# Kernel tuning notes

Hardware: AMD Instinct MI355X
Metric: run time of the kernel (lower is better)

The kernel has to match this reference:

```python
import jax, jax.numpy as jnp
import numpy as np

N, PAIR, M, D, O, R = 4096, 2, 64, 128, 128, 2
MAX_DEG = 32


def setup_inputs() -> dict:
    key = jax.random.key(0)
    k1, k2, k3, k4, k5, k6 = jax.random.split(key, 6)
    node_features = jax.random.normal(k1, (N, PAIR, M, D), dtype=jnp.float32)
    deg = jax.random.randint(k2, (N,), 0, MAX_DEG, dtype=jnp.int32)
    # per-relation Linear params (stored as [in, out]) and self-loop Linear
    W_r = jax.random.normal(k3, (R, D, O), dtype=jnp.float32) / np.sqrt(D)
    b_r = jax.random.normal(k4, (R, O), dtype=jnp.float32) * 0.01
    W0 = jax.random.normal(k5, (D, O), dtype=jnp.float32) / np.sqrt(D)
    b0 = jax.random.normal(k6, (O,), dtype=jnp.float32) * 0.01
    return {"node_features": node_features, "deg": deg, "W_r": W_r,
            "b_r": b_r, "W0": W0, "b0": b0}


def reference(node_features, deg, W_r, b_r, W0, b0):
    # Original: for each relation r, for each neighbor, adds W_r(x_i);
    # i.e. sum_r deg_i * (x_i @ W_r + b_r) = deg_i * (x_i @ sum_r W_r + sum_r b_r)
    Wsum = W_r.sum(axis=0)          # [D, O]
    bsum = b_r.sum(axis=0)          # [O]
    rel = jnp.einsum('npmd,do->npmo', node_features, Wsum) + bsum
    self_term = jnp.einsum('npmd,do->npmo', node_features, W0) + b0
    d = deg.astype(node_features.dtype)[:, None, None, None]
    h = jax.nn.relu(d * rel + self_term)  # [N, 2, M, O]
    # edge representation: mm(h_i, h_j.T) per entity -> [N, M, M]
    out = jnp.einsum('nmo,nko->nmk', h[:, 0], h[:, 1])
    return out
```

## Files before the change

kernel.cpp:

```cpp
#include <hip/hip_runtime.h>
#include <hip/hip_bf16.h>


typedef __attribute__((ext_vector_type(8))) short bf16x8;
typedef __attribute__((ext_vector_type(4))) float f32x4;

__device__ __forceinline__ unsigned int pkbf(float a, float b) {
    union { __hip_bfloat162 h; unsigned int u; } v;
    v.h = __float22bfloat162_rn(float2{a, b});
    return v.u;
}

__global__ __launch_bounds__(256) void build_weights(
    const float* __restrict__ W_r,
    const float* __restrict__ b_r,
    const float* __restrict__ W0,
    const float* __restrict__ b0,
    unsigned short* __restrict__ wfrag,
    float* __restrict__ call)
{
    int t = blockIdx.x * blockDim.x + threadIdx.x;
    int lane = t & 63;
    int ks = (t >> 6) & 3;
    int ct = (t >> 8) & 7;
    int d  = (t >> 11) & 31;
    int o = ct * 16 + (lane & 15);
    int kbase = ks * 32 + (lane >> 4) * 8;
    unsigned int* dst = (unsigned int*)(wfrag + (size_t)t * 8);
#pragma unroll
    for (int j = 0; j < 4; ++j) {
        int k0 = kbase + 2 * j;
        float wA = (float)d * (W_r[k0 * 128 + o] + W_r[128 * 128 + k0 * 128 + o]) + W0[k0 * 128 + o];
        float wB = (float)d * (W_r[(k0 + 1) * 128 + o] + W_r[128 * 128 + (k0 + 1) * 128 + o]) + W0[(k0 + 1) * 128 + o];
        dst[j] = pkbf(wA, wB);
    }
    if (t < 32 * 128) {
        int dd = t >> 7, oo = t & 127;
        call[t] = (float)dd * (b_r[oo] + b_r[128 + oo]) + b0[oo];
    }
}

__global__ __launch_bounds__(256) void edge_kernel(
    const float* __restrict__ x,
    const int* __restrict__ deg,
    const unsigned short* __restrict__ wfrag,
    const float* __restrict__ call,
    float* __restrict__ out)
{
    __shared__ unsigned short hlds[16384];
    char* const ldsb = (char*)hlds;

    const int n = blockIdx.x;
    const int tid = threadIdx.x;
    const int wave = tid >> 6;
    const int lane = tid & 63;
    const int l15 = lane & 15;
    const int lhi = lane >> 4;
    const int d = deg[n];

    const float* xn = x + (size_t)n * (2 * 64 * 128);
    const char* wsrc = (const char*)(wfrag + (size_t)d * (8 * 4 * 64 * 8));
    const float* cd = call + d * 128;

    f32x4 wst[8];
#pragma unroll
    for (int i = 0; i < 8; ++i)
        wst[i] = *(const f32x4*)(wsrc + i * 4096 + tid * 16);

    const int rbase = wave * 32;
    bf16x8 afrag[2][4];
    f32x4 xraw[2][4][2];
#pragma unroll
    for (int rt = 0; rt < 2; ++rt) {
        const float* rowp = xn + (size_t)(rbase + rt * 16 + l15) * 128;
#pragma unroll
        for (int ks = 0; ks < 4; ++ks) {
            const f32x4* p = (const f32x4*)(rowp + ks * 32 + lhi * 8);
            xraw[rt][ks][0] = p[0];
            xraw[rt][ks][1] = p[1];
        }
    }

#pragma unroll
    for (int i = 0; i < 8; ++i)
        *(f32x4*)(ldsb + i * 4096 + tid * 16) = wst[i];

#pragma unroll
    for (int rt = 0; rt < 2; ++rt)
#pragma unroll
        for (int ks = 0; ks < 4; ++ks) {
            f32x4 a0 = xraw[rt][ks][0];
            f32x4 a1 = xraw[rt][ks][1];
            union { bf16x8 v; unsigned int u[4]; } f;
            f.u[0] = pkbf(a0.x, a0.y);
            f.u[1] = pkbf(a0.z, a0.w);
            f.u[2] = pkbf(a1.x, a1.y);
            f.u[3] = pkbf(a1.z, a1.w);
            afrag[rt][ks] = f.v;
        }

    __syncthreads();

    f32x4 ccA = *(const f32x4*)(cd + 0 * 16 + lhi * 4);
    f32x4 ccB = *(const f32x4*)(cd + 1 * 16 + lhi * 4);
#pragma unroll
    for (int p = 0; p < 4; ++p) {
        const int ct0 = 2 * p, ct1 = 2 * p + 1;
        bf16x8 bf0[4], bf1[4];
#pragma unroll
        for (int ks = 0; ks < 4; ++ks) {
            bf0[ks] = *(const bf16x8*)(ldsb + ct0 * 4096 + ks * 1024 + lane * 16);
            bf1[ks] = *(const bf16x8*)(ldsb + ct1 * 4096 + ks * 1024 + lane * 16);
        }
        f32x4 acc0[2] = {{0.f,0.f,0.f,0.f},{0.f,0.f,0.f,0.f}};
        f32x4 acc1[2] = {{0.f,0.f,0.f,0.f},{0.f,0.f,0.f,0.f}};
#pragma unroll
        for (int ks = 0; ks < 4; ++ks) {
#pragma unroll
            for (int rt = 0; rt < 2; ++rt) {
                acc0[rt] = __builtin_amdgcn_mfma_f32_16x16x32_bf16(bf0[ks], afrag[rt][ks], acc0[rt], 0, 0, 0);
                acc1[rt] = __builtin_amdgcn_mfma_f32_16x16x32_bf16(bf1[ks], afrag[rt][ks], acc1[rt], 0, 0, 0);
            }
        }
        const int ctn = (p < 3) ? (2 * p + 2) : 0;
        f32x4 ccA_n = *(const f32x4*)(cd + ctn * 16 + lhi * 4);
        f32x4 ccB_n = *(const f32x4*)(cd + (ctn + 1) * 16 + lhi * 4);

        __syncthreads();

#pragma unroll
        for (int rt = 0; rt < 2; ++rt) {
            const int m = rbase + rt * 16 + l15;
            const int slot = ((lhi >> 1) ^ ((m >> 2) & 1));
            {
                float h0v = fmaxf(acc0[rt][0] + ccA.x, 0.f);
                float h1v = fmaxf(acc0[rt][1] + ccA.y, 0.f);
                float h2v = fmaxf(acc0[rt][2] + ccA.z, 0.f);
                float h3v = fmaxf(acc0[rt][3] + ccA.w, 0.f);
                union { unsigned int u[2]; unsigned long long ull; } pk;
                pk.u[0] = pkbf(h0v, h1v);
                pk.u[1] = pkbf(h2v, h3v);
                *(unsigned long long*)(ldsb + ct0 * 4096 + m * 32 + slot * 16 + (lhi & 1) * 8) = pk.ull;
            }
            {
                float h0v = fmaxf(acc1[rt][0] + ccB.x, 0.f);
                float h1v = fmaxf(acc1[rt][1] + ccB.y, 0.f);
                float h2v = fmaxf(acc1[rt][2] + ccB.z, 0.f);
                float h3v = fmaxf(acc1[rt][3] + ccB.w, 0.f);
                union { unsigned int u[2]; unsigned long long ull; } pk;
                pk.u[0] = pkbf(h0v, h1v);
                pk.u[1] = pkbf(h2v, h3v);
                *(unsigned long long*)(ldsb + ct1 * 4096 + m * 32 + slot * 16 + (lhi & 1) * 8) = pk.ull;
            }
        }
        ccA = ccA_n;
        ccB = ccB_n;
    }
    __syncthreads();

    const int mrow = wave * 16 + l15;
    bf16x8 hb[4];
#pragma unroll
    for (int ks = 0; ks < 4; ++ks) {
        const int ct = ks * 2 + (lhi >> 1);
        const int s  = (lhi & 1) ^ ((mrow >> 2) & 1);
        hb[ks] = *(const bf16x8*)(ldsb + ct * 4096 + mrow * 32 + s * 16);
    }
    float* outn = out + (size_t)n * 4096;
#pragma unroll
    for (int qt = 0; qt < 4; ++qt) {
        const int qrow = 64 + qt * 16 + l15;
        f32x4 acc = {0.f, 0.f, 0.f, 0.f};
#pragma unroll
        for (int ks = 0; ks < 4; ++ks) {
            const int ct = ks * 2 + (lhi >> 1);
            const int s  = (lhi & 1) ^ ((qrow >> 2) & 1);
            bf16x8 ha = *(const bf16x8*)(ldsb + ct * 4096 + qrow * 32 + s * 16);
            acc = __builtin_amdgcn_mfma_f32_16x16x32_bf16(ha, hb[ks], acc, 0, 0, 0);
        }
        *(f32x4*)(outn + mrow * 64 + qt * 16 + lhi * 4) = acc;
    }
}

extern "C" void kernel_launch(void* const* d_in, const int* in_sizes, int n_in,
                              void* d_out, int out_size, void* d_ws, size_t ws_size,
                              hipStream_t stream) {
    const float* x   = (const float*)d_in[0];
    const int*   deg = (const int*)d_in[1];
    const float* W_r = (const float*)d_in[2];
    const float* b_r = (const float*)d_in[3];
    const float* W0  = (const float*)d_in[4];
    const float* b0  = (const float*)d_in[5];
    float* out = (float*)d_out;

    unsigned short* wfrag = (unsigned short*)d_ws;
    float* call = (float*)((unsigned short*)d_ws + 32 * 8 * 4 * 64 * 8);

    build_weights<<<256, 256, 0, stream>>>(W_r, b_r, W0, b0, wfrag, call);
    edge_kernel<<<4096, 256, 0, stream>>>(x, deg, wfrag, call, out);
}
```

Baseline: 76.49 us.

## Process four nodes per block with software-pipelined prefetch of next node's inputs

Each block now handles four consecutive nodes in a loop, prefetching the next node's x rows and degree-specific weight fragments into registers while computing the current node, then writing them to a separate weight LDS buffer. Separate LDS regions for weights and the hidden tile remove the mid-loop barrier that the shared buffer previously required. The grid shrinks fourfold and launch bounds request two blocks per CU, trading higher register pressure and 64KB LDS per block for latency hiding across nodes.

```diff
diff --git a/kernel.cpp b/kernel.cpp
--- a/kernel.cpp
+++ b/kernel.cpp
@@ -40,145 +40,146 @@
     }
 }
 
-__global__ __launch_bounds__(256) void edge_kernel(
+__global__ __launch_bounds__(256, 2) void edge_kernel(
     const float* __restrict__ x,
     const int* __restrict__ deg,
     const unsigned short* __restrict__ wfrag,
     const float* __restrict__ call,
     float* __restrict__ out)
 {
-    __shared__ unsigned short hlds[16384];
-    char* const ldsb = (char*)hlds;
-
-    const int n = blockIdx.x;
+    __shared__ char wlds[32768];
+    __shared__ char hlds[32768];
+
     const int tid = threadIdx.x;
     const int wave = tid >> 6;
     const int lane = tid & 63;
     const int l15 = lane & 15;
     const int lhi = lane >> 4;
-    const int d = deg[n];
-
-    const float* xn = x + (size_t)n * (2 * 64 * 128);
-    const char* wsrc = (const char*)(wfrag + (size_t)d * (8 * 4 * 64 * 8));
-    const float* cd = call + d * 128;
-
-    f32x4 wst[8];
-#pragma unroll
-    for (int i = 0; i < 8; ++i)
-        wst[i] = *(const f32x4*)(wsrc + i * 4096 + tid * 16);
-
     const int rbase = wave * 32;
-    bf16x8 afrag[2][4];
+    const int b4 = blockIdx.x * 4;
+
+    int dg[4];
+#pragma unroll
+    for (int j = 0; j < 4; ++j) dg[j] = deg[b4 + j];
+
     f32x4 xraw[2][4][2];
-#pragma unroll
-    for (int rt = 0; rt < 2; ++rt) {
-        const float* rowp = xn + (size_t)(rbase + rt * 16 + l15) * 128;
-#pragma unroll
-        for (int ks = 0; ks < 4; ++ks) {
-            const f32x4* p = (const f32x4*)(rowp + ks * 32 + lhi * 8);
-            xraw[rt][ks][0] = p[0];
-            xraw[rt][ks][1] = p[1];
-        }
-    }
-
-#pragma unroll
-    for (int i = 0; i < 8; ++i)
-        *(f32x4*)(ldsb + i * 4096 + tid * 16) = wst[i];
-
-#pragma unroll
-    for (int rt = 0; rt < 2; ++rt)
-#pragma unroll
-        for (int ks = 0; ks < 4; ++ks) {
-            f32x4 a0 = xraw[rt][ks][0];
-            f32x4 a1 = xraw[rt][ks][1];
-            union { bf16x8 v; unsigned int u[4]; } f;
-            f.u[0] = pkbf(a0.x, a0.y);
-            f.u[1] = pkbf(a0.z, a0.w);
-            f.u[2] = pkbf(a1.x, a1.y);
-            f.u[3] = pkbf(a1.z, a1.w);
-            afrag[rt][ks] = f.v;
-        }
-
+    auto issue_x = [&](int n) {
+        const float* xn = x + (size_t)n * (2 * 64 * 128);
+#pragma unroll
+        for (int rt = 0; rt < 2; ++rt) {
+            const float* rowp = xn + (size_t)(rbase + rt * 16 + l15) * 128;
+#pragma unroll
+            for (int ks = 0; ks < 4; ++ks) {
+                const f32x4* p = (const f32x4*)(rowp + ks * 32 + lhi * 8);
+                xraw[rt][ks][0] = p[0];
+                xraw[rt][ks][1] = p[1];
+            }
+        }
+    };
+
+    {
+        const char* wsrc = (const char*)(wfrag + (size_t)dg[0] * (8 * 4 * 64 * 8));
+        f32x4 w0[8];
+#pragma unroll
+        for (int i = 0; i < 8; ++i)
+            w0[i] = *(const f32x4*)(wsrc + i * 4096 + tid * 16);
+        issue_x(b4);
+#pragma unroll
+        for (int i = 0; i < 8; ++i)
+            *(f32x4*)(wlds + i * 4096 + tid * 16) = w0[i];
+    }
     __syncthreads();
 
-    f32x4 ccA = *(const f32x4*)(cd + 0 * 16 + lhi * 4);
-    f32x4 ccB = *(const f32x4*)(cd + 1 * 16 + lhi * 4);
-#pragma unroll
-    for (int p = 0; p < 4; ++p) {
-        const int ct0 = 2 * p, ct1 = 2 * p + 1;
-        bf16x8 bf0[4], bf1[4];
-#pragma unroll
-        for (int ks = 0; ks < 4; ++ks) {
-            bf0[ks] = *(const bf16x8*)(ldsb + ct0 * 4096 + ks * 1024 + lane * 16);
-            bf1[ks] = *(const bf16x8*)(ldsb + ct1 * 4096 + ks * 1024 + lane * 16);
-        }
-        f32x4 acc0[2] = {{0.f,0.f,0.f,0.f},{0.f,0.f,0.f,0.f}};
-        f32x4 acc1[2] = {{0.f,0.f,0.f,0.f},{0.f,0.f,0.f,0.f}};
-#pragma unroll
-        for (int ks = 0; ks < 4; ++ks) {
+    for (int j = 0; j < 4; ++j) {
+        const float* cd = call + dg[j] * 128;
+
+        f32x4 ccv[8];
+#pragma unroll
+        for (int ct = 0; ct < 8; ++ct)
+            ccv[ct] = *(const f32x4*)(cd + ct * 16 + lhi * 4);
+
+        bf16x8 afrag[2][4];
+#pragma unroll
+        for (int rt = 0; rt < 2; ++rt)
+#pragma unroll
+            for (int ks = 0; ks < 4; ++ks) {
+                f32x4 a0 = xraw[rt][ks][0];
+                f32x4 a1 = xraw[rt][ks][1];
+                union { bf16x8 v; unsigned int u[4]; } f;
+                f.u[0] = pkbf(a0.x, a0.y);
+                f.u[1] = pkbf(a0.z, a0.w);
+                f.u[2] = pkbf(a1.x, a1.y);
+                f.u[3] = pkbf(a1.z, a1.w);
+                afrag[rt][ks] = f.v;
+            }
+
+        f32x4 wst[8];
+        if (j < 3) {
+            const char* wsrc = (const char*)(wfrag + (size_t)dg[j + 1] * (8 * 4 * 64 * 8));
+#pragma unroll
+            for (int i = 0; i < 8; ++i)
+                wst[i] = *(const f32x4*)(wsrc + i * 4096 + tid * 16);
+            issue_x(b4 + j + 1);
+        }
+
+#pragma unroll
+        for (int ct = 0; ct < 8; ++ct) {
+            bf16x8 bfrag[4];
+#pragma unroll
+            for (int ks = 0; ks < 4; ++ks)
+                bfrag[ks] = *(const bf16x8*)(wlds + ct * 4096 + ks * 1024 + lane * 16);
+            f32x4 acc[2] = {{0.f,0.f,0.f,0.f},{0.f,0.f,0.f,0.f}};
+#pragma unroll
+            for (int ks = 0; ks < 4; ++ks)
+#pragma unroll
+                for (int rt = 0; rt < 2; ++rt)
+                    acc[rt] = __builtin_amdgcn_mfma_f32_16x16x32_bf16(bfrag[ks], afrag[rt][ks], acc[rt], 0, 0, 0);
+            const f32x4 cc4 = ccv[ct];
 #pragma unroll
             for (int rt = 0; rt < 2; ++rt) {
-                acc0[rt] = __builtin_amdgcn_mfma_f32_16x16x32_bf16(bf0[ks], afrag[rt][ks], acc0[rt], 0, 0, 0);
-                acc1[rt] = __builtin_amdgcn_mfma_f32_16x16x32_bf16(bf1[ks], afrag[rt][ks], acc1[rt], 0, 0, 0);
-            }
-        }
-        const int ctn = (p < 3) ? (2 * p + 2) : 0;
-        f32x4 ccA_n = *(const f32x4*)(cd + ctn * 16 + lhi * 4);
-        f32x4 ccB_n = *(const f32x4*)(cd + (ctn + 1) * 16 + lhi * 4);
-
-        __syncthreads();
-
-#pragma unroll
-        for (int rt = 0; rt < 2; ++rt) {
-            const int m = rbase + rt * 16 + l15;
-            const int slot = ((lhi >> 1) ^ ((m >> 2) & 1));
-            {
-                float h0v = fmaxf(acc0[rt][0] + ccA.x, 0.f);
-                float h1v = fmaxf(acc0[rt][1] + ccA.y, 0.f);
-                float h2v = fmaxf(acc0[rt][2] + ccA.z, 0.f);
-                float h3v = fmaxf(acc0[rt][3] + ccA.w, 0.f);
+                const int m = rbase + rt * 16 + l15;
+                const int slot = (lhi >> 1) ^ ((m >> 2) & 1);
+                float h0v = fmaxf(acc[rt][0] + cc4.x, 0.f);
+                float h1v = fmaxf(acc[rt][1] + cc4.y, 0.f);
+                float h2v = fmaxf(acc[rt][2] + cc4.z, 0.f);
+                float h3v = fmaxf(acc[rt][3] + cc4.w, 0.f);
                 union { unsigned int u[2]; unsigned long long ull; } pk;
                 pk.u[0] = pkbf(h0v, h1v);
                 pk.u[1] = pkbf(h2v, h3v);
-                *(unsigned long long*)(ldsb + ct0 * 4096 + m * 32 + slot * 16 + (lhi & 1) * 8) = pk.ull;
-            }
-            {
-                float h0v = fmaxf(acc1[rt][0] + ccB.x, 0.f);
-                float h1v = fmaxf(acc1[rt][1] + ccB.y, 0.f);
-                float h2v = fmaxf(acc1[rt][2] + ccB.z, 0.f);
-                float h3v = fmaxf(acc1[rt][3] + ccB.w, 0.f);
-                union { unsigned int u[2]; unsigned long long ull; } pk;
-                pk.u[0] = pkbf(h0v, h1v);
-                pk.u[1] = pkbf(h2v, h3v);
-                *(unsigned long long*)(ldsb + ct1 * 4096 + m * 32 + slot * 16 + (lhi & 1) * 8) = pk.ull;
-            }
-        }
-        ccA = ccA_n;
-        ccB = ccB_n;
-    }
-    __syncthreads();
-
-    const int mrow = wave * 16 + l15;
-    bf16x8 hb[4];
-#pragma unroll
-    for (int ks = 0; ks < 4; ++ks) {
-        const int ct = ks * 2 + (lhi >> 1);
-        const int s  = (lhi & 1) ^ ((mrow >> 2) & 1);
-        hb[ks] = *(const bf16x8*)(ldsb + ct * 4096 + mrow * 32 + s * 16);
-    }
-    float* outn = out + (size_t)n * 4096;
-#pragma unroll
-    for (int qt = 0; qt < 4; ++qt) {
-        const int qrow = 64 + qt * 16 + l15;
-        f32x4 acc = {0.f, 0.f, 0.f, 0.f};
+                *(unsigned long long*)(hlds + ct * 4096 + m * 32 + slot * 16 + (lhi & 1) * 8) = pk.ull;
+            }
+        }
+        __syncthreads();
+
+        const int mrow = wave * 16 + l15;
+        bf16x8 hb[4];
 #pragma unroll
         for (int ks = 0; ks < 4; ++ks) {
             const int ct = ks * 2 + (lhi >> 1);
-            const int s  = (lhi & 1) ^ ((qrow >> 2) & 1);
-            bf16x8 ha = *(const bf16x8*)(ldsb + ct * 4096 + qrow * 32 + s * 16);
-            acc = __builtin_amdgcn_mfma_f32_16x16x32_bf16(ha, hb[ks], acc, 0, 0, 0);
-        }
-        *(f32x4*)(outn + mrow * 64 + qt * 16 + lhi * 4) = acc;
+            const int s  = (lhi & 1) ^ ((mrow >> 2) & 1);
+            hb[ks] = *(const bf16x8*)(hlds + ct * 4096 + mrow * 32 + s * 16);
+        }
+        float* outn = out + (size_t)(b4 + j) * 4096;
+#pragma unroll
+        for (int qt = 0; qt < 4; ++qt) {
+            const int qrow = 64 + qt * 16 + l15;
+            f32x4 acc = {0.f, 0.f, 0.f, 0.f};
+#pragma unroll
+            for (int ks = 0; ks < 4; ++ks) {
+                const int ct = ks * 2 + (lhi >> 1);
+                const int s  = (lhi & 1) ^ ((qrow >> 2) & 1);
+                bf16x8 ha = *(const bf16x8*)(hlds + ct * 4096 + qrow * 32 + s * 16);
+                acc = __builtin_amdgcn_mfma_f32_16x16x32_bf16(ha, hb[ks], acc, 0, 0, 0);
+            }
+            *(f32x4*)(outn + mrow * 64 + qt * 16 + lhi * 4) = acc;
+        }
+
+        if (j < 3) {
+#pragma unroll
+            for (int i = 0; i < 8; ++i)
+                *(f32x4*)(wlds + i * 4096 + tid * 16) = wst[i];
+        }
+        __syncthreads();
     }
 }
 
@@ -197,5 +198,5 @@
     float* call = (float*)((unsigned short*)d_ws + 32 * 8 * 4 * 64 * 8);
 
     build_weights<<<256, 256, 0, stream>>>(W_r, b_r, W0, b0, wfrag, call);
-    edge_kernel<<<4096, 256, 0, stream>>>(x, deg, wfrag, call, out);
-}
+    edge_kernel<<<1024, 256, 0, stream>>>(x, deg, wfrag, call, out);
+}
```

Result: slower. 83.79 us (+9.5%).
